# Kernel optimization log

Measured on AMD Instinct MI355X. Metric: run time of the kernel, lower is better.

Reference implementation:

```python
import jax, jax.numpy as jnp
import numpy as np

SCALE = 0.25  # matches torch forward default scale=1/4 (static: determines output shape)


def _cubic(x):
    # MATLAB bicubic kernel, a = -0.5
    a = np.abs(x)
    a2 = a * a
    a3 = a2 * a
    c1 = (a <= 1).astype(np.float32)
    c2 = ((a > 1) & (a <= 2)).astype(np.float32)
    return (1.5 * a3 - 2.5 * a2 + 1.0) * c1 + (-0.5 * a3 + 2.5 * a2 - 4.0 * a + 2.0) * c2


def _contrib_1d(in_len, out_len, scale):
    # Faithful numpy port of bicubic_imresize.contribute for one axis.
    kw = 4.0 / scale if scale < 1 else 4.0
    x = np.arange(1, out_len + 1, dtype=np.float32)
    u = x / scale + 0.5 * (1.0 - 1.0 / scale)
    left = np.floor(u - kw / 2.0)
    P = int(np.ceil(kw) + 2)
    ind = left[:, None] + np.arange(P, dtype=np.float32)[None, :]   # [out_len, P]
    mid = u[:, None] - ind
    w = scale * _cubic(mid * scale) if scale < 1 else _cubic(mid)
    w = w / w.sum(axis=1, keepdims=True)
    ind = np.clip(ind, 1.0, float(in_len))
    kill = (w[0] == 0)  # torch prunes columns where the FIRST row weight is zero
    w = w[:, ~kill].astype(np.float32)
    idx = ind[:, ~kill].astype(np.int64) - 1  # 0-based
    return w, idx


def setup_inputs() -> dict:
    key = jax.random.key(0)
    return {"input": jax.random.normal(key, (8, 3, 1024, 1024), dtype=jnp.float32)}


def reference(input):
    b, c, h, w_in = input.shape
    oh, ow = int(h * SCALE), int(w_in * SCALE)
    w0_np, i0_np = _contrib_1d(h, oh, SCALE)      # rows: [oh, P0]
    w1_np, i1_np = _contrib_1d(w_in, ow, SCALE)   # cols: [ow, P1]
    w0 = jnp.asarray(w0_np)
    w1 = jnp.asarray(w1_np)
    i0 = jnp.asarray(i0_np)
    i1 = jnp.asarray(i1_np)
    # vertical pass: gather rows then weighted reduce over taps
    rows = input[:, :, i0, :]                          # [b, c, oh, P0, w_in]
    tmp = jnp.einsum('bcopw,op->bcow', rows, w0)       # [b, c, oh, w_in]
    # horizontal pass
    cols = tmp[:, :, :, i1]                            # [b, c, oh, ow, P1]
    out = jnp.einsum('bcowp,wp->bcow', cols, w1)       # [b, c, oh, ow]
    return out
```

## Files before the change

### kernel.cpp

```cpp
#include <hip/hip_runtime.h>

#define IN_H 1024
#define IN_W 1024
#define OUT_H 256
#define OUT_W 256
#define G 4
#define ROWS (4*G + 12)

__constant__ float WTAP[16] = {
    -0.001708984375f, -0.010986328125f, -0.018310546875f, -0.011962890625f,
     0.022705078125f,  0.097412109375f,  0.181884765625f,  0.240966796875f,
     0.240966796875f,  0.181884765625f,  0.097412109375f,  0.022705078125f,
    -0.011962890625f, -0.018310546875f, -0.010986328125f, -0.001708984375f
};

#define SWZ(x) ((x) + ((x) >> 3))
#define LDS_ROW (IN_W + IN_W / 8)

__global__ __launch_bounds__(256)
void bicubic_fused_kernel(const float* __restrict__ in, float* __restrict__ out) {
    const int t   = threadIdx.x;
    const int bc  = blockIdx.x / (OUT_H / G);
    const int og  = blockIdx.x % (OUT_H / G);
    const int oh0 = og * G;

    __shared__ float vrow[G][LDS_ROW];

    const float* src = in + (size_t)bc * IN_H * IN_W;

    float4 acc[G];
#pragma unroll
    for (int i = 0; i < G; ++i) acc[i] = make_float4(0.f, 0.f, 0.f, 0.f);

#pragma unroll
    for (int r = 0; r < ROWS; ++r) {
        int y = oh0 * 4 + r - 6;
        y = min(max(y, 0), IN_H - 1);
        const float4 v = *(const float4*)(src + (size_t)y * IN_W + 4 * t);
#pragma unroll
        for (int i = 0; i < G; ++i) {
            const int j = r - 4 * i;
            if (j >= 0 && j < 16) {
                const float w = WTAP[j];
                acc[i].x = fmaf(w, v.x, acc[i].x);
                acc[i].y = fmaf(w, v.y, acc[i].y);
                acc[i].z = fmaf(w, v.z, acc[i].z);
                acc[i].w = fmaf(w, v.w, acc[i].w);
            }
        }
    }

    {
        const int x0 = 4 * t;
        const int a0 = SWZ(x0);
#pragma unroll
        for (int i = 0; i < G; ++i) {
            vrow[i][a0 + 0] = acc[i].x;
            vrow[i][a0 + 1] = acc[i].y;
            vrow[i][a0 + 2] = acc[i].z;
            vrow[i][a0 + 3] = acc[i].w;
        }
    }
    __syncthreads();

#pragma unroll
    for (int i = 0; i < G; ++i) {
        float s = 0.f;
#pragma unroll
        for (int j = 0; j < 16; ++j) {
            int x = 4 * t + j - 6;
            x = min(max(x, 0), IN_W - 1);
            s = fmaf(WTAP[j], vrow[i][SWZ(x)], s);
        }
        out[((size_t)bc * OUT_H + oh0 + i) * OUT_W + t] = s;
    }
}

extern "C" void kernel_launch(void* const* d_in, const int* in_sizes, int n_in,
                              void* d_out, int out_size, void* d_ws, size_t ws_size,
                              hipStream_t stream) {
    const float* in = (const float*)d_in[0];
    float* out = (float*)d_out;
    const int nbc = in_sizes[0] / (IN_H * IN_W);
    dim3 grid(nbc * (OUT_H / G));
    dim3 block(256);
    bicubic_fused_kernel<<<grid, block, 0, stream>>>(in, out);
}
```

Measured before the change: 147.2 us.

## Double output rows per block and use guarded padded LDS with vector reads

Raises the number of output rows per block from 4 to 8. This lowers the vertical halo overhead, going from 28 input rows per 4 outputs to 44 per 8. It also replaces the swizzled LDS layout with a padded pitch holding replicated edge guard cells, so the horizontal pass can read taps as float4 without clamping. Stores become float2 and occupancy is hinted at 3 blocks. The risks are more registers for the 8 float4 accumulators, more LDS per block, and possible bank conflicts from the strided float4 LDS reads.

After: 146.8 us. About the same (-0.3%).

```diff
diff --git a/kernel.cpp b/kernel.cpp
--- a/kernel.cpp
+++ b/kernel.cpp
@@ -4,8 +4,10 @@
 #define IN_W 1024
 #define OUT_H 256
 #define OUT_W 256
-#define G 4
+#define G 8
 #define ROWS (4*G + 12)
+#define GUARD_L 6
+#define PITCH 1040
 
 __constant__ float WTAP[16] = {
     -0.001708984375f, -0.010986328125f, -0.018310546875f, -0.011962890625f,
@@ -14,17 +16,14 @@
     -0.011962890625f, -0.018310546875f, -0.010986328125f, -0.001708984375f
 };
 
-#define SWZ(x) ((x) + ((x) >> 3))
-#define LDS_ROW (IN_W + IN_W / 8)
-
-__global__ __launch_bounds__(256)
+__global__ __launch_bounds__(256, 3)
 void bicubic_fused_kernel(const float* __restrict__ in, float* __restrict__ out) {
     const int t   = threadIdx.x;
     const int bc  = blockIdx.x / (OUT_H / G);
     const int og  = blockIdx.x % (OUT_H / G);
     const int oh0 = og * G;
 
-    __shared__ float vrow[G][LDS_ROW];
+    __shared__ float vrow[G][PITCH];
 
     const float* src = in + (size_t)bc * IN_H * IN_W;
 
@@ -50,27 +49,35 @@
         }
     }
 
-    {
-        const int x0 = 4 * t;
-        const int a0 = SWZ(x0);
 #pragma unroll
-        for (int i = 0; i < G; ++i) {
-            vrow[i][a0 + 0] = acc[i].x;
-            vrow[i][a0 + 1] = acc[i].y;
-            vrow[i][a0 + 2] = acc[i].z;
-            vrow[i][a0 + 3] = acc[i].w;
-        }
+    for (int i = 0; i < G; ++i) {
+        float2* p = (float2*)&vrow[i][GUARD_L + 4 * t];
+        p[0] = make_float2(acc[i].x, acc[i].y);
+        p[1] = make_float2(acc[i].z, acc[i].w);
+    }
+    if (t == 0) {
+#pragma unroll
+        for (int i = 0; i < G; ++i)
+            for (int k = 0; k < GUARD_L; ++k) vrow[i][k] = acc[i].x;
+    }
+    if (t == 255) {
+#pragma unroll
+        for (int i = 0; i < G; ++i)
+            for (int k = GUARD_L + IN_W; k < PITCH; ++k) vrow[i][k] = acc[i].w;
     }
     __syncthreads();
 
 #pragma unroll
     for (int i = 0; i < G; ++i) {
+        const float4* q = (const float4*)&vrow[i][4 * t];
         float s = 0.f;
 #pragma unroll
-        for (int j = 0; j < 16; ++j) {
-            int x = 4 * t + j - 6;
-            x = min(max(x, 0), IN_W - 1);
-            s = fmaf(WTAP[j], vrow[i][SWZ(x)], s);
+        for (int k = 0; k < 4; ++k) {
+            const float4 v = q[k];
+            s = fmaf(WTAP[4 * k + 0], v.x, s);
+            s = fmaf(WTAP[4 * k + 1], v.y, s);
+            s = fmaf(WTAP[4 * k + 2], v.z, s);
+            s = fmaf(WTAP[4 * k + 3], v.w, s);
         }
         out[((size_t)bc * OUT_H + oh0 + i) * OUT_W + t] = s;
     }
```
